# Performance work log

Measured on AMD Instinct MI355X. Metric: run time of the kernel, lower is better.

## Reference

```python
import jax, jax.numpy as jnp
import numpy as np

G = 0.001
EPS = 1e-6


def setup_inputs() -> dict:
    key = jax.random.key(0)
    k1, k2 = jax.random.split(key)
    B, N, D = 8, 4096, 3
    q = jax.random.normal(k1, (B, N, D), dtype=jnp.float32)
    m = jax.random.uniform(k2, (N,), dtype=jnp.float32)
    return {"q": q, "m": m}


def reference(q, m):
    # q: (B, N, D), m: (N,)
    N = q.shape[-2]
    diff = q[:, :, None, :] - q[:, None, :, :]          # (B, N, N, D)
    dist = jnp.sqrt(jnp.sum(diff * diff, axis=-1) + EPS)  # (B, N, N)
    mass_matrix = m[:, None] * m[None, :]                # (N, N)
    V = -G * mass_matrix / dist                          # (B, N, N)
    # zero the diagonal (self-interaction), matching fill_(0.0)
    off_diag = 1.0 - jnp.eye(N, dtype=q.dtype)
    V = V * off_diag
    return jnp.sum(V, axis=(-1, -2)) / 2.0               # (B,)
```

## Files before the change

kernel.cpp:

```cpp
#include <hip/hip_runtime.h>

typedef float v4f __attribute__((ext_vector_type(4)));

#define BLK 256
#define IPT 4
#define TI (BLK * IPT)
#define TJ 64
#define JBT (TI / TJ)
#define G_CONST 0.001f
#define EPS_CONST 1e-6f

__global__ __launch_bounds__(BLK, 5)
void grav_kernel(const float* __restrict__ q, const float* __restrict__ m,
                 float* __restrict__ out, int N) {
  const int b   = blockIdx.z;
  const int tid = threadIdx.x;

  int rel = blockIdx.x;
  int a = 0;
  while (rel >= JBT * (a + 1)) { rel -= JBT * (a + 1); ++a; }
  const int jt   = rel;
  const bool diag = (jt >= JBT * a);
  const int i0 = a * TI;
  const int j0 = jt * TJ;

  __shared__ float xs[TJ], ys[TJ], zs[TJ], sjs[TJ], ms[TJ];
  __shared__ float wsum[4];

  const float* qb = q + (size_t)b * N * 3;

  if (tid < TJ) {
    const int j = j0 + tid;
    const float x = qb[3 * j + 0];
    const float y = qb[3 * j + 1];
    const float z = qb[3 * j + 2];
    xs[tid]  = x;
    ys[tid]  = y;
    zs[tid]  = z;
    sjs[tid] = fmaf(x, x, fmaf(y, y, z * z));
    ms[tid]  = m[j];
  }

  float xi[IPT], yi[IPT], zi[IPT], txi[IPT], tyi[IPT], tzi[IPT], se[IPT], mi[IPT];
#pragma unroll
  for (int s = 0; s < IPT; ++s) {
    const int i = i0 + s * BLK + tid;
    xi[s] = qb[3 * i + 0];
    yi[s] = qb[3 * i + 1];
    zi[s] = qb[3 * i + 2];
    txi[s] = -2.f * xi[s];
    tyi[s] = -2.f * yi[s];
    tzi[s] = -2.f * zi[s];
    se[s] = fmaf(xi[s], xi[s], fmaf(yi[s], yi[s], fmaf(zi[s], zi[s], EPS_CONST)));
    mi[s] = m[i];
  }

  __syncthreads();

  float acc[IPT] = {};

  if (diag) {
#pragma unroll 2
    for (int k = 0; k < TJ; k += 4) {
      const v4f xj = *(const v4f*)&xs[k];
      const v4f yj = *(const v4f*)&ys[k];
      const v4f zj = *(const v4f*)&zs[k];
      const v4f mj = *(const v4f*)&ms[k];
#pragma unroll
      for (int s = 0; s < IPT; ++s) {
#pragma unroll
        for (int u = 0; u < 4; ++u) {
          const float dx = xi[s] - xj[u];
          const float dy = yi[s] - yj[u];
          const float dz = zi[s] - zj[u];
          const float r2 = fmaf(dx, dx, fmaf(dy, dy, fmaf(dz, dz, EPS_CONST)));
          acc[s] = fmaf(mj[u], __builtin_amdgcn_rsqf(r2), acc[s]);
        }
      }
    }
  } else {
#pragma unroll 2
    for (int k = 0; k < TJ; k += 4) {
      const v4f xj = *(const v4f*)&xs[k];
      const v4f yj = *(const v4f*)&ys[k];
      const v4f zj = *(const v4f*)&zs[k];
      const v4f sj = *(const v4f*)&sjs[k];
      const v4f mj = *(const v4f*)&ms[k];
#pragma unroll
      for (int s = 0; s < IPT; ++s) {
#pragma unroll
        for (int u = 0; u < 4; ++u) {
          float t = se[s] + sj[u];
          t = fmaf(txi[s], xj[u], t);
          t = fmaf(tyi[s], yj[u], t);
          t = fmaf(tzi[s], zj[u], t);
          acc[s] = fmaf(mj[u], __builtin_amdgcn_rsqf(t), acc[s]);
        }
      }
    }
  }

  float tsum = 0.f;
#pragma unroll
  for (int s = 0; s < IPT; ++s) {
    const int i = i0 + s * BLK + tid;
    float h = acc[s];
    if (diag && i >= j0 && i < j0 + TJ) h -= mi[s] * __builtin_amdgcn_rsqf(EPS_CONST);
    tsum += mi[s] * h;
  }

#pragma unroll
  for (int off = 32; off > 0; off >>= 1) tsum += __shfl_down(tsum, off);
  const int wid  = tid >> 6;
  const int lane = tid & 63;
  if (lane == 0) wsum[wid] = tsum;
  __syncthreads();
  if (tid == 0) {
    const float s = (wsum[0] + wsum[1]) + (wsum[2] + wsum[3]);
    const float scale = diag ? (-0.5f * G_CONST) : (-G_CONST);
    atomicAdd(out + b, s * scale);
  }
}

extern "C" void kernel_launch(void* const* d_in, const int* in_sizes, int n_in,
                              void* d_out, int out_size, void* d_ws, size_t ws_size,
                              hipStream_t stream) {
  const float* q = (const float*)d_in[0];
  const float* m = (const float*)d_in[1];
  float* out = (float*)d_out;

  const int N = in_sizes[1];
  const int B = in_sizes[0] / (N * 3);

  hipMemsetAsync(out, 0, (size_t)out_size * sizeof(float), stream);

  const int nti = N / TI;
  const int bpb = JBT * nti * (nti + 1) / 2;
  dim3 grid(bpb, 1, B);
  grav_kernel<<<grid, BLK, 0, stream>>>(q, m, out, N);
}
```

Before: 31.32 us.

## Drop expanded-distance path, use direct differences with larger i-tiles and smaller j-tiles

Removes the off-diagonal path that expanded |xi-xj|^2 as si+sj-2xi·xj and uses the direct difference form for every tile. This frees per-i registers, which pays for doubling the i-points per thread to 8 while halving the j-tile to 32 and raising the occupancy hint. The direct form costs one more VALU op per pair but avoids the cancellation error of the expanded form. The retiling also changes the triangular block count and the LDS reuse per load.

```diff
diff --git a/kernel.cpp b/kernel.cpp
--- a/kernel.cpp
+++ b/kernel.cpp
@@ -3,14 +3,14 @@
 typedef float v4f __attribute__((ext_vector_type(4)));
 
 #define BLK 256
-#define IPT 4
+#define IPT 8
 #define TI (BLK * IPT)
-#define TJ 64
+#define TJ 32
 #define JBT (TI / TJ)
 #define G_CONST 0.001f
 #define EPS_CONST 1e-6f
 
-__global__ __launch_bounds__(BLK, 5)
+__global__ __launch_bounds__(BLK, 6)
 void grav_kernel(const float* __restrict__ q, const float* __restrict__ m,
                  float* __restrict__ out, int N) {
   const int b   = blockIdx.z;
@@ -24,34 +24,26 @@
   const int i0 = a * TI;
   const int j0 = jt * TJ;
 
-  __shared__ float xs[TJ], ys[TJ], zs[TJ], sjs[TJ], ms[TJ];
+  __shared__ float xs[TJ], ys[TJ], zs[TJ], ms[TJ];
   __shared__ float wsum[4];
 
   const float* qb = q + (size_t)b * N * 3;
 
   if (tid < TJ) {
     const int j = j0 + tid;
-    const float x = qb[3 * j + 0];
-    const float y = qb[3 * j + 1];
-    const float z = qb[3 * j + 2];
-    xs[tid]  = x;
-    ys[tid]  = y;
-    zs[tid]  = z;
-    sjs[tid] = fmaf(x, x, fmaf(y, y, z * z));
-    ms[tid]  = m[j];
+    xs[tid] = qb[3 * j + 0];
+    ys[tid] = qb[3 * j + 1];
+    zs[tid] = qb[3 * j + 2];
+    ms[tid] = m[j];
   }
 
-  float xi[IPT], yi[IPT], zi[IPT], txi[IPT], tyi[IPT], tzi[IPT], se[IPT], mi[IPT];
+  float xi[IPT], yi[IPT], zi[IPT], mi[IPT];
 #pragma unroll
   for (int s = 0; s < IPT; ++s) {
     const int i = i0 + s * BLK + tid;
     xi[s] = qb[3 * i + 0];
     yi[s] = qb[3 * i + 1];
     zi[s] = qb[3 * i + 2];
-    txi[s] = -2.f * xi[s];
-    tyi[s] = -2.f * yi[s];
-    tzi[s] = -2.f * zi[s];
-    se[s] = fmaf(xi[s], xi[s], fmaf(yi[s], yi[s], fmaf(zi[s], zi[s], EPS_CONST)));
     mi[s] = m[i];
   }
 
@@ -59,43 +51,20 @@
 
   float acc[IPT] = {};
 
-  if (diag) {
-#pragma unroll 2
-    for (int k = 0; k < TJ; k += 4) {
-      const v4f xj = *(const v4f*)&xs[k];
-      const v4f yj = *(const v4f*)&ys[k];
-      const v4f zj = *(const v4f*)&zs[k];
-      const v4f mj = *(const v4f*)&ms[k];
+  for (int k = 0; k < TJ; k += 4) {
+    const v4f xj = *(const v4f*)&xs[k];
+    const v4f yj = *(const v4f*)&ys[k];
+    const v4f zj = *(const v4f*)&zs[k];
+    const v4f mj = *(const v4f*)&ms[k];
 #pragma unroll
-      for (int s = 0; s < IPT; ++s) {
+    for (int s = 0; s < IPT; ++s) {
 #pragma unroll
-        for (int u = 0; u < 4; ++u) {
-          const float dx = xi[s] - xj[u];
-          const float dy = yi[s] - yj[u];
-          const float dz = zi[s] - zj[u];
-          const float r2 = fmaf(dx, dx, fmaf(dy, dy, fmaf(dz, dz, EPS_CONST)));
-          acc[s] = fmaf(mj[u], __builtin_amdgcn_rsqf(r2), acc[s]);
-        }
-      }
-    }
-  } else {
-#pragma unroll 2
-    for (int k = 0; k < TJ; k += 4) {
-      const v4f xj = *(const v4f*)&xs[k];
-      const v4f yj = *(const v4f*)&ys[k];
-      const v4f zj = *(const v4f*)&zs[k];
-      const v4f sj = *(const v4f*)&sjs[k];
-      const v4f mj = *(const v4f*)&ms[k];
-#pragma unroll
-      for (int s = 0; s < IPT; ++s) {
-#pragma unroll
-        for (int u = 0; u < 4; ++u) {
-          float t = se[s] + sj[u];
-          t = fmaf(txi[s], xj[u], t);
-          t = fmaf(tyi[s], yj[u], t);
-          t = fmaf(tzi[s], zj[u], t);
-          acc[s] = fmaf(mj[u], __builtin_amdgcn_rsqf(t), acc[s]);
-        }
+      for (int u = 0; u < 4; ++u) {
+        const float dx = xi[s] - xj[u];
+        const float dy = yi[s] - yj[u];
+        const float dz = zi[s] - zj[u];
+        const float r2 = fmaf(dx, dx, fmaf(dy, dy, fmaf(dz, dz, EPS_CONST)));
+        acc[s] = fmaf(mj[u], __builtin_amdgcn_rsqf(r2), acc[s]);
       }
     }
   }
@@ -105,7 +74,8 @@
   for (int s = 0; s < IPT; ++s) {
     const int i = i0 + s * BLK + tid;
     float h = acc[s];
-    if (diag && i >= j0 && i < j0 + TJ) h -= mi[s] * __builtin_amdgcn_rsqf(EPS_CONST);
+    if (diag && i >= j0 && i < j0 + TJ)
+      h -= mi[s] * __builtin_amdgcn_rsqf(EPS_CONST);
     tsum += mi[s] * h;
   }
 
```

New measurement: 35.50 us. 13.4% more time.
